# Kernel optimization log

Measured on AMD Instinct MI355X. Metric: run time of the kernel, lower is better.

Reference implementation:

```python
import jax, jax.numpy as jnp
import numpy as np

N_NODES = 100000
N_EDGES = 600000
HID = 128
CH_OUT = 3


def setup_inputs() -> dict:
    key = jax.random.key(0)
    ks = jax.random.split(key, 16)
    s = 0.05  # small init to keep tanh in its linear-ish range
    inp = {
        "x": jax.random.normal(ks[0], (N_NODES, HID), dtype=jnp.float32),
        "pos": jax.random.normal(ks[1], (N_NODES, 3), dtype=jnp.float32),
        "edge_index": jax.random.randint(ks[2], (2, N_EDGES), 0, N_NODES, dtype=jnp.int32),
        "fe_w1": jax.random.normal(ks[3], (2 * HID + 1, HID), dtype=jnp.float32) * s,
        "fe_b1": jnp.zeros((HID,), jnp.float32),
        "fe_w2": jax.random.normal(ks[4], (HID, HID), dtype=jnp.float32) * s,
        "fe_b2": jnp.zeros((HID,), jnp.float32),
        "finf_w": jax.random.normal(ks[5], (HID, 1), dtype=jnp.float32) * s,
        "finf_b": jnp.zeros((1,), jnp.float32),
        "fh_w1": jax.random.normal(ks[6], (2 * HID, HID), dtype=jnp.float32) * s,
        "fh_b1": jnp.zeros((HID,), jnp.float32),
        "fh_w2": jax.random.normal(ks[7], (HID, HID), dtype=jnp.float32) * s,
        "fh_b2": jnp.zeros((HID,), jnp.float32),
        "l1_w": jax.random.normal(ks[8], (HID, HID), dtype=jnp.float32) * s,
        "l1_b": jnp.zeros((HID,), jnp.float32),
        "l2_w": jax.random.normal(ks[9], (HID, HID), dtype=jnp.float32) * s,
        "l2_b": jnp.zeros((HID,), jnp.float32),
        "l3_w": jax.random.normal(ks[10], (HID, HID), dtype=jnp.float32) * s,
        "l3_b": jnp.zeros((HID,), jnp.float32),
        "l4_w": jax.random.normal(ks[11], (HID, HID), dtype=jnp.float32) * s,
        "l4_b": jnp.zeros((HID,), jnp.float32),
        "l5_w": jax.random.normal(ks[12], (HID, CH_OUT), dtype=jnp.float32) * s,
        "l5_b": jnp.zeros((CH_OUT,), jnp.float32),
    }
    return inp


def reference(x, pos, edge_index, fe_w1, fe_b1, fe_w2, fe_b2, finf_w, finf_b,
              fh_w1, fh_b1, fh_w2, fh_b2, l1_w, l1_b, l2_w, l2_b, l3_w, l3_b,
              l4_w, l4_b, l5_w, l5_b):
    e_st, e_end = edge_index[0], edge_index[1]
    # dists = ||(pos_i - pos_j)^2||_2  (norm of the squared difference, as in source)
    d = pos[e_st] - pos[e_end]                                  # [E, 3]
    dists = jnp.linalg.norm(jnp.square(d), axis=1, keepdims=True)  # [E, 1]
    # edge MLP f_e
    tmp = jnp.concatenate([x[e_st], x[e_end], dists], axis=1)   # [E, 2H+1]
    m_ij = jnp.tanh(tmp @ fe_w1 + fe_b1)
    m_ij = jnp.tanh(m_ij @ fe_w2 + fe_b2)                        # [E, H]
    # gating f_inf
    e_ij = jnp.tanh(m_ij @ finf_w + finf_b)                      # [E, 1]
    # scatter-sum to source nodes (index_add on edge_index[0])
    m_i = jax.ops.segment_sum(e_ij * m_ij, e_st, num_segments=x.shape[0])  # [N, H]
    # node update f_h with residual
    h = jnp.concatenate([x, m_i], axis=1)                        # [N, 2H]
    x = x + (jnp.tanh(h @ fh_w1 + fh_b1) @ fh_w2 + fh_b2)
    # dense head (dropout p=0.0 is identity)
    lrelu = lambda v: jax.nn.leaky_relu(v, negative_slope=0.01)
    x = lrelu(x @ l1_w + l1_b)
    x = lrelu(x @ l2_w + l2_b)
    x = lrelu(x @ l3_w + l3_b)
    x = lrelu(x @ l4_w + l4_b)
    return x @ l5_w + l5_b
```

## Files before the change

### kernel.cpp

```cpp
#include <hip/hip_runtime.h>
#include <math.h>

#define HID 128

typedef unsigned short u16;
typedef __attribute__((ext_vector_type(8))) short bfrag;
typedef __attribute__((ext_vector_type(4))) float f32x4;
typedef __attribute__((ext_vector_type(8))) unsigned short u16x8;
typedef __attribute__((ext_vector_type(4))) unsigned short u16x4;

__device__ __forceinline__ float fast_tanh(float v) {
    v = fminf(15.0f, fmaxf(-15.0f, v));
    float e = __expf(2.0f * v);
    float r = __builtin_amdgcn_rcpf(e + 1.0f);
    return 1.0f - 2.0f * r;
}

__device__ __forceinline__ u16 f2b(float f) {
    union { float f; unsigned int u; } v;
    v.f = f;
    unsigned int u = v.u;
    return (u16)((u + 0x7FFFu + ((u >> 16) & 1u)) >> 16);
}
__device__ __forceinline__ float b2f(u16 b) {
    union { unsigned int u; float f; } v;
    v.u = ((unsigned int)b) << 16;
    return v.f;
}
__device__ __forceinline__ float bits2f(unsigned u) {
    union { unsigned u; float f; } v; v.u = u; return v.f;
}

__global__ void __launch_bounds__(256) prep_x(const float* __restrict__ x,
                                              u16* __restrict__ xb) {
    int i = blockIdx.x * 256 + threadIdx.x;
    const float4 v0 = *(const float4*)(x + (size_t)i * 8);
    const float4 v1 = *(const float4*)(x + (size_t)i * 8 + 4);
    u16x8 o = { f2b(v0.x), f2b(v0.y), f2b(v0.z), f2b(v0.w),
                f2b(v1.x), f2b(v1.y), f2b(v1.z), f2b(v1.w) };
    *(u16x8*)(xb + (size_t)i * 8) = o;
}

__global__ void __launch_bounds__(256) prep_weights(
    const float* __restrict__ w1, const float* __restrict__ fh1,
    const float* __restrict__ w2, const float* __restrict__ fh2,
    const float* __restrict__ l1, const float* __restrict__ l2,
    const float* __restrict__ l3, const float* __restrict__ l4,
    u16* __restrict__ w1t, u16* __restrict__ fh1t,
    u16* __restrict__ w2t, u16* __restrict__ fh2t,
    u16* __restrict__ l1t, u16* __restrict__ l2t,
    u16* __restrict__ l3t, u16* __restrict__ l4t)
{
    int b = blockIdx.x, t = threadIdx.x;
    const float* src; u16* dst; int K;
    if (b < 256) {
        K = 256;
        if (b < 128) { src = w1;  dst = w1t; }
        else         { src = fh1; dst = fh1t; b -= 128; }
    } else {
        K = 128;
        int s = (b - 256) >> 6; b = (b - 256) & 63;
        switch (s) {
            case 0:  src = w2;  dst = w2t;  break;
            case 1:  src = fh2; dst = fh2t; break;
            case 2:  src = l1;  dst = l1t;  break;
            case 3:  src = l2;  dst = l2t;  break;
            case 4:  src = l3;  dst = l3t;  break;
            default: src = l4;  dst = l4t;  break;
        }
    }
    int idx = b * 256 + t;
    int k = idx >> 7, n = idx & 127;
    dst[(size_t)n * K + k] = f2b(src[(size_t)k * 128 + n]);
}

__global__ void __launch_bounds__(256) hist_kernel(const int* __restrict__ est,
                                                   int* __restrict__ cnt, int E) {
    int e = blockIdx.x * 256 + threadIdx.x;
    if (e < E) atomicAdd(&cnt[est[e]], 1);
}

__global__ void __launch_bounds__(256) scan1(const int* __restrict__ cnt,
                                             int* __restrict__ scanout,
                                             int* __restrict__ partial, int N) {
    __shared__ int s[256];
    int t = threadIdx.x, b = blockIdx.x, i = b * 256 + t;
    int v = (i < N) ? cnt[i] : 0;
    s[t] = v; __syncthreads();
#pragma unroll
    for (int d = 1; d < 256; d <<= 1) {
        int add = (t >= d) ? s[t - d] : 0;
        __syncthreads();
        s[t] += add;
        __syncthreads();
    }
    if (i < N) scanout[i] = s[t] - v;
    if (t == 255) partial[b] = s[255];
}

__global__ void __launch_bounds__(512) scan2(int* __restrict__ partial, int NB) {
    __shared__ int s[512];
    int t = threadIdx.x;
    int v = (t < NB) ? partial[t] : 0;
    s[t] = v; __syncthreads();
#pragma unroll
    for (int d = 1; d < 512; d <<= 1) {
        int add = (t >= d) ? s[t - d] : 0;
        __syncthreads();
        s[t] += add;
        __syncthreads();
    }
    if (t < NB) partial[t] = s[t] - v;
}

__global__ void __launch_bounds__(256) scan3(const int* __restrict__ scanout,
                                             const int* __restrict__ partial,
                                             int* __restrict__ offs,
                                             int* __restrict__ cur, int N, int E) {
    int t = threadIdx.x, b = blockIdx.x, i = b * 256 + t;
    if (i < N) { int o = scanout[i] + partial[b]; offs[i] = o; cur[i] = o; }
    if (i == 0) offs[N] = E;
}

__global__ void __launch_bounds__(256) reorder_kernel(const int* __restrict__ est,
                                                      const int* __restrict__ eend,
                                                      int* __restrict__ cur,
                                                      int* __restrict__ est_s,
                                                      int* __restrict__ eend_s, int E) {
    int e = blockIdx.x * 256 + threadIdx.x;
    if (e < E) {
        int s = est[e];
        int p = atomicAdd(&cur[s], 1);
        est_s[p]  = s;
        eend_s[p] = eend[e];
    }
}

template<int KD>
__device__ __forceinline__ void gemm_k(const u16* sbuf, const u16* __restrict__ wt,
                                       int w, int l16, int l4g, f32x4 (&acc)[2][2]) {
    const int RS = KD * 2;
#pragma unroll
    for (int k0 = 0; k0 < KD; k0 += 32) {
        const int kb = k0 * 2 + l4g * 16;
        bfrag a0 = *(const bfrag*)((const char*)sbuf +
                    (unsigned)((l16 * RS + kb) ^ ((l16 & 7) << 4)));
        bfrag a1 = *(const bfrag*)((const char*)sbuf +
                    (unsigned)(((16 + l16) * RS + kb) ^ ((l16 & 7) << 4)));
        bfrag b0 = *(const bfrag*)((const char*)wt + (size_t)(32 * w + l16) * RS + kb);
        bfrag b1 = *(const bfrag*)((const char*)wt + (size_t)(32 * w + 16 + l16) * RS + kb);
        acc[0][0] = __builtin_amdgcn_mfma_f32_16x16x32_bf16(a0, b0, acc[0][0], 0, 0, 0);
        acc[0][1] = __builtin_amdgcn_mfma_f32_16x16x32_bf16(a0, b1, acc[0][1], 0, 0, 0);
        acc[1][0] = __builtin_amdgcn_mfma_f32_16x16x32_bf16(a1, b0, acc[1][0], 0, 0, 0);
        acc[1][1] = __builtin_amdgcn_mfma_f32_16x16x32_bf16(a1, b1, acc[1][1], 0, 0, 0);
    }
}

template<int KD>
__device__ __forceinline__ void gemm_sw(const u16* act, const u16* __restrict__ wt,
                                        int w, int l16, int l4g, f32x4 (&acc)[2][2]) {
    const int RS = KD * 2;
#pragma unroll
    for (int k0 = 0; k0 < KD; k0 += 32) {
        const int kb = k0 * 2 + l4g * 16;
        bfrag wa0 = *(const bfrag*)((const char*)wt + (size_t)(32 * w + l16) * RS + kb);
        bfrag wa1 = *(const bfrag*)((const char*)wt + (size_t)(32 * w + 16 + l16) * RS + kb);
        bfrag be0 = *(const bfrag*)((const char*)act +
                    (unsigned)((l16 * RS + kb) ^ ((l16 & 7) << 4)));
        bfrag be1 = *(const bfrag*)((const char*)act +
                    (unsigned)(((16 + l16) * RS + kb) ^ ((l16 & 7) << 4)));
        acc[0][0] = __builtin_amdgcn_mfma_f32_16x16x32_bf16(wa0, be0, acc[0][0], 0, 0, 0);
        acc[0][1] = __builtin_amdgcn_mfma_f32_16x16x32_bf16(wa0, be1, acc[0][1], 0, 0, 0);
        acc[1][0] = __builtin_amdgcn_mfma_f32_16x16x32_bf16(wa1, be0, acc[1][0], 0, 0, 0);
        acc[1][1] = __builtin_amdgcn_mfma_f32_16x16x32_bf16(wa1, be1, acc[1][1], 0, 0, 0);
    }
}

__global__ void __launch_bounds__(256, 2)
egc_edge_csr(const u16* __restrict__ xb, const float* __restrict__ pos,
             const int* __restrict__ est_s, const int* __restrict__ eend_s,
             const u16* __restrict__ w1t, const float* __restrict__ w1last,
             const float* __restrict__ b1, const u16* __restrict__ w2t,
             const float* __restrict__ b2, const float* __restrict__ fw,
             const float* __restrict__ fb, u16* __restrict__ g,
             float* __restrict__ ev, int n_tiles)
{
    __shared__ __attribute__((aligned(16))) u16 a_sh[2][32 * 256];
    __shared__ __attribute__((aligned(16))) u16 m1_sh[32 * 128];
    __shared__ float red[32][17];
    __shared__ float dist_l[2][32];

    const int t = threadIdx.x, lane = t & 63, w = t >> 6;
    const int l16 = lane & 15, l4g = lane >> 4;
    const unsigned swz = (unsigned)((l16 & 7) << 4);

    bfrag wa10[8], wa11[8], w2f0[4], w2f1[4];
#pragma unroll
    for (int i = 0; i < 8; ++i) {
        int kb = i * 64 + l4g * 16;
        wa10[i] = *(const bfrag*)((const char*)w1t + (size_t)(32 * w + l16) * 512 + kb);
        wa11[i] = *(const bfrag*)((const char*)w1t + (size_t)(32 * w + 16 + l16) * 512 + kb);
    }
#pragma unroll
    for (int i = 0; i < 4; ++i) {
        int kb = i * 64 + l4g * 16;
        w2f0[i] = *(const bfrag*)((const char*)w2t + (size_t)(32 * w + l16) * 256 + kb);
        w2f1[i] = *(const bfrag*)((const char*)w2t + (size_t)(32 * w + 16 + l16) * 256 + kb);
    }
    float w1l_r[2][4], b1_r[2][4], b2_r[2][4], fw_r[2][4];
#pragma unroll
    for (int mi = 0; mi < 2; ++mi)
#pragma unroll
        for (int rg = 0; rg < 4; ++rg) {
            int n = 32 * w + 16 * mi + l4g * 4 + rg;
            w1l_r[mi][rg] = w1last[n];
            b1_r[mi][rg]  = b1[n];
            b2_r[mi][rg]  = b2[n];
            fw_r[mi][rg]  = fw[n];
        }
    const float fbv = fb[0];

    float4 sv0, sv1, sv2, sv3;
    float pax = 0, pay = 0, paz = 0, pbx = 0, pby = 0, pbz = 0;

#define EDGE_ISSUE(TILE) do {                                                  \
        int e0_ = (TILE) * 32;                                                 \
        { int f_ = t;       int e_ = f_ >> 5, q_ = f_ & 31; int ge_ = e0_ + e_;\
          int nd_ = (q_ < 16) ? est_s[ge_] : eend_s[ge_];                      \
          sv0 = *(const float4*)(xb + (size_t)nd_ * 128 + (q_ & 15) * 8); }    \
        { int f_ = t + 256; int e_ = f_ >> 5, q_ = f_ & 31; int ge_ = e0_ + e_;\
          int nd_ = (q_ < 16) ? est_s[ge_] : eend_s[ge_];                      \
          sv1 = *(const float4*)(xb + (size_t)nd_ * 128 + (q_ & 15) * 8); }    \
        { int f_ = t + 512; int e_ = f_ >> 5, q_ = f_ & 31; int ge_ = e0_ + e_;\
          int nd_ = (q_ < 16) ? est_s[ge_] : eend_s[ge_];                      \
          sv2 = *(const float4*)(xb + (size_t)nd_ * 128 + (q_ & 15) * 8); }    \
        { int f_ = t + 768; int e_ = f_ >> 5, q_ = f_ & 31; int ge_ = e0_ + e_;\
          int nd_ = (q_ < 16) ? est_s[ge_] : eend_s[ge_];                      \
          sv3 = *(const float4*)(xb + (size_t)nd_ * 128 + (q_ & 15) * 8); }    \
        if (t < 32) {                                                          \
            int ge_ = e0_ + t;                                                 \
            int a_ = est_s[ge_], b_ = eend_s[ge_];                             \
            pax = pos[a_ * 3]; pay = pos[a_ * 3 + 1]; paz = pos[a_ * 3 + 2];   \
            pbx = pos[b_ * 3]; pby = pos[b_ * 3 + 1]; pbz = pos[b_ * 3 + 2];   \
        }                                                                      \
    } while (0)

#define EDGE_COMMIT(BUF) do {                                                  \
        { int f_ = t;       int e_ = f_ >> 5, q_ = f_ & 31;                    \
          unsigned by_ = (unsigned)(e_ * 512 + q_ * 16) ^ (unsigned)((e_ & 7) << 4); \
          *(float4*)((char*)a_sh[BUF] + by_) = sv0; }                          \
        { int f_ = t + 256; int e_ = f_ >> 5, q_ = f_ & 31;                    \
          unsigned by_ = (unsigned)(e_ * 512 + q_ * 16) ^ (unsigned)((e_ & 7) << 4); \
          *(float4*)((char*)a_sh[BUF] + by_) = sv1; }                          \
        { int f_ = t + 512; int e_ = f_ >> 5, q_ = f_ & 31;                    \
          unsigned by_ = (unsigned)(e_ * 512 + q_ * 16) ^ (unsigned)((e_ & 7) << 4); \
          *(float4*)((char*)a_sh[BUF] + by_) = sv2; }                          \
        { int f_ = t + 768; int e_ = f_ >> 5, q_ = f_ & 31;                    \
          unsigned by_ = (unsigned)(e_ * 512 + q_ * 16) ^ (unsigned)((e_ & 7) << 4); \
          *(float4*)((char*)a_sh[BUF] + by_) = sv3; }                          \
        if (t < 32) {                                                          \
            float dx_ = pax - pbx, dy_ = pay - pby, dz_ = paz - pbz;           \
            dx_ *= dx_; dy_ *= dy_; dz_ *= dz_;                                \
            dist_l[BUF][t] = sqrtf(dx_ * dx_ + dy_ * dy_ + dz_ * dz_);         \
        }                                                                      \
    } while (0)

    int tile = blockIdx.x;
    EDGE_ISSUE(tile);
    int buf = 0;

    if (tile < n_tiles)
    while (true) {
        EDGE_COMMIT(buf);
        __syncthreads();
        int next = tile + gridDim.x;
        if (next < n_tiles) EDGE_ISSUE(next);
        const int e0 = tile * 32;

        {
            f32x4 acc[2][2] = {};
#pragma unroll
            for (int i = 0; i < 8; ++i) {
                int kb = i * 64 + l4g * 16;
                bfrag be0 = *(const bfrag*)((const char*)a_sh[buf] +
                            ((unsigned)(l16 * 512 + kb) ^ swz));
                bfrag be1 = *(const bfrag*)((const char*)a_sh[buf] +
                            ((unsigned)((16 + l16) * 512 + kb) ^ swz));
                acc[0][0] = __builtin_amdgcn_mfma_f32_16x16x32_bf16(wa10[i], be0, acc[0][0], 0, 0, 0);
                acc[0][1] = __builtin_amdgcn_mfma_f32_16x16x32_bf16(wa10[i], be1, acc[0][1], 0, 0, 0);
                acc[1][0] = __builtin_amdgcn_mfma_f32_16x16x32_bf16(wa11[i], be0, acc[1][0], 0, 0, 0);
                acc[1][1] = __builtin_amdgcn_mfma_f32_16x16x32_bf16(wa11[i], be1, acc[1][1], 0, 0, 0);
            }
            float de0 = dist_l[buf][l16];
            float de1 = dist_l[buf][16 + l16];
#pragma unroll
            for (int mi = 0; mi < 2; ++mi)
#pragma unroll
                for (int ni = 0; ni < 2; ++ni) {
                    float de = ni ? de1 : de0;
                    u16x4 pk;
#pragma unroll
                    for (int rg = 0; rg < 4; ++rg) {
                        float v = fast_tanh(acc[mi][ni][rg] + de * w1l_r[mi][rg] + b1_r[mi][rg]);
                        pk[rg] = f2b(v);
                    }
                    unsigned byte = ((unsigned)((16 * ni + l16) * 256 +
                                     (32 * w + 16 * mi + l4g * 4) * 2)) ^ swz;
                    *(u16x4*)((char*)m1_sh + byte) = pk;
                }
        }
        __syncthreads();

        {
            f32x4 acc[2][2] = {};
#pragma unroll
            for (int i = 0; i < 4; ++i) {
                int kb = i * 64 + l4g * 16;
                bfrag me0 = *(const bfrag*)((const char*)m1_sh +
                            ((unsigned)(l16 * 256 + kb) ^ swz));
                bfrag me1 = *(const bfrag*)((const char*)m1_sh +
                            ((unsigned)((16 + l16) * 256 + kb) ^ swz));
                acc[0][0] = __builtin_amdgcn_mfma_f32_16x16x32_bf16(w2f0[i], me0, acc[0][0], 0, 0, 0);
                acc[0][1] = __builtin_amdgcn_mfma_f32_16x16x32_bf16(w2f0[i], me1, acc[0][1], 0, 0, 0);
                acc[1][0] = __builtin_amdgcn_mfma_f32_16x16x32_bf16(w2f1[i], me0, acc[1][0], 0, 0, 0);
                acc[1][1] = __builtin_amdgcn_mfma_f32_16x16x32_bf16(w2f1[i], me1, acc[1][1], 0, 0, 0);
            }
            float part0 = 0.0f, part1 = 0.0f;
#pragma unroll
            for (int mi = 0; mi < 2; ++mi)
#pragma unroll
                for (int ni = 0; ni < 2; ++ni) {
                    u16x4 pk;
                    float ps = 0.0f;
#pragma unroll
                    for (int rg = 0; rg < 4; ++rg) {
                        float v = fast_tanh(acc[mi][ni][rg] + b2_r[mi][rg]);
                        ps += v * fw_r[mi][rg];
                        pk[rg] = f2b(v);
                    }
                    if (ni) part1 += ps; else part0 += ps;
                    int dstrow = e0 + 16 * ni + l16;
                    *(u16x4*)(g + (size_t)dstrow * 128 + (32 * w + 16 * mi + l4g * 4)) = pk;
                }
            red[l16][w * 4 + l4g]      = part0;
            red[16 + l16][w * 4 + l4g] = part1;
        }
        __syncthreads();

        if (t < 32) {
            float s = 0.0f;
#pragma unroll
            for (int j = 0; j < 16; ++j) s += red[t][j];
            ev[e0 + t] = fast_tanh(s + fbv);
        }

        tile = next; buf ^= 1;
        if (tile >= n_tiles) break;
    }
#undef EDGE_ISSUE
#undef EDGE_COMMIT
}

__global__ void __launch_bounds__(256, 8)
gather_seq(const u16* __restrict__ g, const float* __restrict__ ev,
           const int* __restrict__ offs, u16* __restrict__ m_i)
{
    const int lane = threadIdx.x & 63;
    const int half = lane >> 5;
    const int l32  = lane & 31;
    const int n = blockIdx.x * 4 + (threadIdx.x >> 6);
    const int beg = offs[n], end = offs[n + 1];
    float a0 = 0.0f, a1 = 0.0f, a2 = 0.0f, a3 = 0.0f;
    for (int e = beg + half; e < end; e += 2) {
        uint2 v = *(const uint2*)(g + (size_t)e * 128 + l32 * 4);
        float ee = ev[e];
        a0 += ee * bits2f(v.x << 16);
        a1 += ee * bits2f(v.x & 0xFFFF0000u);
        a2 += ee * bits2f(v.y << 16);
        a3 += ee * bits2f(v.y & 0xFFFF0000u);
    }
    a0 += __shfl_xor(a0, 32);
    a1 += __shfl_xor(a1, 32);
    a2 += __shfl_xor(a2, 32);
    a3 += __shfl_xor(a3, 32);
    if (half == 0) {
        uint2 o;
        o.x = (unsigned)f2b(a0) | ((unsigned)f2b(a1) << 16);
        o.y = (unsigned)f2b(a2) | ((unsigned)f2b(a3) << 16);
        *(uint2*)(m_i + (size_t)n * 128 + l32 * 4) = o;
    }
}

__global__ void __launch_bounds__(256, 3)
egc_edge_mfma(const u16* __restrict__ xb, const float* __restrict__ pos,
              const int* __restrict__ est, const int* __restrict__ eend,
              const u16* __restrict__ w1t, const float* __restrict__ w1last,
              const float* __restrict__ b1, const u16* __restrict__ w2t,
              const float* __restrict__ b2, const float* __restrict__ fw,
              const float* __restrict__ fb, float* __restrict__ m_i)
{
    __shared__ __attribute__((aligned(16))) u16 a_sh[32 * 256];
    __shared__ __attribute__((aligned(16))) u16 m1_sh[32 * 128];
    __shared__ float m2_sh[32][132];
    __shared__ float dist_l[32];
    __shared__ float ev_l[32];
    __shared__ int   st_l[32];

    const int t = threadIdx.x;
    const int e0 = blockIdx.x * 32;
    const int lane = t & 63;
    const int w = t >> 6;
    const int l16 = lane & 15, l4g = lane >> 4;

#pragma unroll
    for (int i = 0; i < 4; ++i) {
        int f = t + 256 * i;
        int e = f >> 5, q = f & 31;
        int ge = e0 + e;
        int node = (q < 16) ? est[ge] : eend[ge];
        float4 v = *(const float4*)(xb + (size_t)node * 128 + (q & 15) * 8);
        unsigned byte = (unsigned)(e * 512 + q * 16) ^ (unsigned)((e & 7) << 4);
        *(float4*)((char*)a_sh + byte) = v;
    }
    if (t < 32) {
        int ge = e0 + t;
        int a = est[ge], b = eend[ge];
        st_l[t] = a;
        float dx = pos[a * 3 + 0] - pos[b * 3 + 0];
        float dy = pos[a * 3 + 1] - pos[b * 3 + 1];
        float dz = pos[a * 3 + 2] - pos[b * 3 + 2];
        dx *= dx; dy *= dy; dz *= dz;
        dist_l[t] = sqrtf(dx * dx + dy * dy + dz * dz);
    }
    __syncthreads();

    {
        f32x4 acc[2][2] = {};
        gemm_k<256>(a_sh, w1t, w, l16, l4g, acc);
#pragma unroll
        for (int mi = 0; mi < 2; ++mi)
#pragma unroll
            for (int ni = 0; ni < 2; ++ni) {
                const int col = 32 * w + 16 * ni + l16;
                const float wl = w1last[col], bb = b1[col];
#pragma unroll
                for (int rg = 0; rg < 4; ++rg) {
                    const int row = 16 * mi + l4g * 4 + rg;
                    float v = fast_tanh(acc[mi][ni][rg] + dist_l[row] * wl + bb);
                    unsigned byte = (unsigned)((row * 256 + col * 2) ^ ((row & 7) << 4));
                    *(u16*)((char*)m1_sh + byte) = f2b(v);
                }
            }
    }
    __syncthreads();

    {
        f32x4 acc[2][2] = {};
        gemm_k<128>(m1_sh, w2t, w, l16, l4g, acc);
#pragma unroll
        for (int mi = 0; mi < 2; ++mi)
#pragma unroll
            for (int ni = 0; ni < 2; ++ni) {
                const int col = 32 * w + 16 * ni + l16;
                const float bb = b2[col];
#pragma unroll
                for (int rg = 0; rg < 4; ++rg) {
                    const int row = 16 * mi + l4g * 4 + rg;
                    m2_sh[row][col] = fast_tanh(acc[mi][ni][rg] + bb);
                }
            }
    }
    __syncthreads();

    if (t < 128) {
        int e = t >> 2, p = t & 3;
        float s = 0.0f;
#pragma unroll
        for (int k = 0; k < 32; ++k) s += m2_sh[e][p * 32 + k] * fw[p * 32 + k];
        s += __shfl_xor(s, 1);
        s += __shfl_xor(s, 2);
        if (p == 0) ev_l[e] = fast_tanh(s + fb[0]);
    }
    __syncthreads();

    {
        int e = t >> 3, l8 = t & 7;
        float ev = ev_l[e];
        size_t base = (size_t)st_l[e] * HID + l8;
#pragma unroll
        for (int i = 0; i < 16; ++i)
            unsafeAtomicAdd(m_i + base + 8 * i, ev * m2_sh[e][l8 + 8 * i]);
    }
}

#define NODE_LAYER_SW(SRC, KD, WT, BIAS, DST, ACT)                             \
    {                                                                          \
        f32x4 acc[2][2] = {};                                                  \
        gemm_sw<KD>(SRC, WT, w, l16, l4g, acc);                                \
        float bbr[2][4];                                                       \
        _Pragma("unroll")                                                      \
        for (int mi = 0; mi < 2; ++mi)                                         \
            _Pragma("unroll")                                                  \
            for (int rg = 0; rg < 4; ++rg)                                     \
                bbr[mi][rg] = (BIAS)[32 * w + 16 * mi + l4g * 4 + rg];         \
        _Pragma("unroll")                                                      \
        for (int mi = 0; mi < 2; ++mi)                                         \
            _Pragma("unroll")                                                  \
            for (int ni = 0; ni < 2; ++ni) {                                   \
                const int node = 16 * ni + l16;                                \
                const int ch = 32 * w + 16 * mi + l4g * 4;                     \
                u16x4 pk;                                                      \
                _Pragma("unroll")                                              \
                for (int rg = 0; rg < 4; ++rg) {                               \
                    float v = acc[mi][ni][rg] + bbr[mi][rg];                   \
                    ACT;                                                       \
                    pk[rg] = f2b(v);                                           \
                }                                                              \
                unsigned byte = ((unsigned)(node * 256 + ch * 2)) ^ swz;       \
                *(u16x4*)((char*)(DST) + byte) = pk;                           \
            }                                                                  \
    }

template<bool MIBF16>
__global__ void __launch_bounds__(256, 3)
egc_node_mfma(const u16* __restrict__ xb, const float* __restrict__ xf,
              const void* __restrict__ m_i,
              const u16* __restrict__ fh1t, const float* __restrict__ hb1,
              const u16* __restrict__ fh2t, const float* __restrict__ hb2,
              const u16* __restrict__ l1t, const float* __restrict__ l1b,
              const u16* __restrict__ l2t, const float* __restrict__ l2b,
              const u16* __restrict__ l3t, const float* __restrict__ l3b,
              const u16* __restrict__ l4t, const float* __restrict__ l4b,
              const float* __restrict__ l5w, const float* __restrict__ l5b,
              float* __restrict__ out)
{
    __shared__ __attribute__((aligned(16))) u16 a_sh[32 * 256];
    __shared__ __attribute__((aligned(16))) u16 bA[32 * 128];
    __shared__ __attribute__((aligned(16))) u16 bB[32 * 128];
    __shared__ float ff[32][132];

    const int t = threadIdx.x;
    const int n0 = blockIdx.x * 32;
    const int lane = t & 63;
    const int w = t >> 6;
    const int l16 = lane & 15, l4g = lane >> 4;
    const unsigned swz = (unsigned)((l16 & 7) << 4);

#pragma unroll
    for (int i = 0; i < 2; ++i) {
        int f = t + 256 * i;
        int n = f >> 4, q = f & 15;
        float4 v = *(const float4*)(xb + (size_t)(n0 + n) * 128 + q * 8);
        unsigned byte = (unsigned)((n * 512 + q * 16) ^ ((n & 7) << 4));
        *(float4*)((char*)a_sh + byte) = v;
    }
    if (MIBF16) {
#pragma unroll
        for (int i = 0; i < 2; ++i) {
            int f = t + 256 * i;
            int n = f >> 4, q = f & 15;
            float4 v = *(const float4*)((const u16*)m_i + (size_t)(n0 + n) * 128 + q * 8);
            unsigned byte = (unsigned)((n * 512 + 256 + q * 16) ^ ((n & 7) << 4));
            *(float4*)((char*)a_sh + byte) = v;
        }
    } else {
#pragma unroll
        for (int i = 0; i < 2; ++i) {
            int f = t + 256 * i;
            int n = f >> 4, q = f & 15;
            const float* src = (const float*)m_i + (size_t)(n0 + n) * 128 + q * 8;
            float4 v0 = *(const float4*)(src);
            float4 v1 = *(const float4*)(src + 4);
            u16x8 o = { f2b(v0.x), f2b(v0.y), f2b(v0.z), f2b(v0.w),
                        f2b(v1.x), f2b(v1.y), f2b(v1.z), f2b(v1.w) };
            unsigned byte = (unsigned)((n * 512 + 256 + q * 16) ^ ((n & 7) << 4));
            *(u16x8*)((char*)a_sh + byte) = o;
        }
    }
    __syncthreads();

    NODE_LAYER_SW(a_sh, 256, fh1t, hb1, bA, { v = fast_tanh(v); })
    __syncthreads();

    {
        f32x4 acc[2][2] = {};
        gemm_sw<128>(bA, fh2t, w, l16, l4g, acc);
        float bbr[2][4];
#pragma unroll
        for (int mi = 0; mi < 2; ++mi)
#pragma unroll
            for (int rg = 0; rg < 4; ++rg)
                bbr[mi][rg] = hb2[32 * w + 16 * mi + l4g * 4 + rg];
#pragma unroll
        for (int mi = 0; mi < 2; ++mi)
#pragma unroll
            for (int ni = 0; ni < 2; ++ni) {
                const int node = 16 * ni + l16;
                const int ch = 32 * w + 16 * mi + l4g * 4;
                float4 xr = *(const float4*)(xf + (size_t)(n0 + node) * 128 + ch);
                u16x4 pk;
                pk[0] = f2b(acc[mi][ni][0] + bbr[mi][0] + xr.x);
                pk[1] = f2b(acc[mi][ni][1] + bbr[mi][1] + xr.y);
                pk[2] = f2b(acc[mi][ni][2] + bbr[mi][2] + xr.z);
                pk[3] = f2b(acc[mi][ni][3] + bbr[mi][3] + xr.w);
                unsigned byte = ((unsigned)(node * 256 + ch * 2)) ^ swz;
                *(u16x4*)((char*)bB + byte) = pk;
            }
    }
    __syncthreads();

    NODE_LAYER_SW(bB, 128, l1t, l1b, bA, { v = v > 0.0f ? v : 0.01f * v; })
    __syncthreads();
    NODE_LAYER_SW(bA, 128, l2t, l2b, bB, { v = v > 0.0f ? v : 0.01f * v; })
    __syncthreads();
    NODE_LAYER_SW(bB, 128, l3t, l3b, bA, { v = v > 0.0f ? v : 0.01f * v; })
    __syncthreads();

    {
        f32x4 acc[2][2] = {};
        gemm_sw<128>(bA, l4t, w, l16, l4g, acc);
        float bbr[2][4];
#pragma unroll
        for (int mi = 0; mi < 2; ++mi)
#pragma unroll
            for (int rg = 0; rg < 4; ++rg)
                bbr[mi][rg] = l4b[32 * w + 16 * mi + l4g * 4 + rg];
#pragma unroll
        for (int mi = 0; mi < 2; ++mi)
#pragma unroll
            for (int ni = 0; ni < 2; ++ni) {
                const int node = 16 * ni + l16;
                const int ch = 32 * w + 16 * mi + l4g * 4;
                float4 o;
                float v0 = acc[mi][ni][0] + bbr[mi][0];
                float v1 = acc[mi][ni][1] + bbr[mi][1];
                float v2 = acc[mi][ni][2] + bbr[mi][2];
                float v3 = acc[mi][ni][3] + bbr[mi][3];
                o.x = v0 > 0.0f ? v0 : 0.01f * v0;
                o.y = v1 > 0.0f ? v1 : 0.01f * v1;
                o.z = v2 > 0.0f ? v2 : 0.01f * v2;
                o.w = v3 > 0.0f ? v3 : 0.01f * v3;
                *(float4*)(&ff[node][ch]) = o;
            }
    }
    __syncthreads();

    if (t < 96) {
        int n = t / 3, cc = t % 3;
        float s = l5b[cc];
#pragma unroll 8
        for (int k = 0; k < HID; ++k) s += ff[n][k] * l5w[k * 3 + cc];
        out[(size_t)(n0 + n) * 3 + cc] = s;
    }
}

extern "C" void kernel_launch(void* const* d_in, const int* in_sizes, int n_in,
                              void* d_out, int out_size, void* d_ws, size_t ws_size,
                              hipStream_t stream)
{
    const float* x      = (const float*)d_in[0];
    const float* pos    = (const float*)d_in[1];
    const int*   eidx   = (const int*)d_in[2];
    const float* fe_w1  = (const float*)d_in[3];
    const float* fe_b1  = (const float*)d_in[4];
    const float* fe_w2  = (const float*)d_in[5];
    const float* fe_b2  = (const float*)d_in[6];
    const float* finf_w = (const float*)d_in[7];
    const float* finf_b = (const float*)d_in[8];
    const float* fh_w1  = (const float*)d_in[9];
    const float* fh_b1  = (const float*)d_in[10];
    const float* fh_w2  = (const float*)d_in[11];
    const float* fh_b2  = (const float*)d_in[12];
    const float* l1w    = (const float*)d_in[13];
    const float* l1b    = (const float*)d_in[14];
    const float* l2w    = (const float*)d_in[15];
    const float* l2b    = (const float*)d_in[16];
    const float* l3w    = (const float*)d_in[17];
    const float* l3b    = (const float*)d_in[18];
    const float* l4w    = (const float*)d_in[19];
    const float* l4b    = (const float*)d_in[20];
    const float* l5w    = (const float*)d_in[21];
    const float* l5b    = (const float*)d_in[22];
    float* out = (float*)d_out;

    const int n_edges = in_sizes[2] / 2;
    const int n_nodes = in_sizes[0] / HID;
    const int nsb     = (n_nodes + 255) / 256;
    const int n_tiles = n_edges / 32;

    char* ws = (char*)d_ws;
    const bool use_csr = (ws_size >= 208800000ULL);

    if (use_csr) {
        u16* g     = (u16*)(ws + 0);
        u16* xb    = (u16*)(ws + 153600000);
        u16* m_i   = (u16*)(ws + 179200000);
        int* est_s  = (int*)(ws + 179200000);
        int* eend_s = (int*)(ws + 181600000);
        u16* w1t  = (u16*)(ws + 204800000);
        u16* w2t  = (u16*)(ws + 204865536);
        u16* fh1t = (u16*)(ws + 204898304);
        u16* fh2t = (u16*)(ws + 204963840);
        u16* l1t  = (u16*)(ws + 204996608);
        u16* l2t  = (u16*)(ws + 205029376);
        u16* l3t  = (u16*)(ws + 205062144);
        u16* l4t  = (u16*)(ws + 205094912);
        int* cnt  = (int*)(ws + 205127680);
        int* offs = (int*)(ws + 205527680);
        int* cur  = (int*)(ws + 205927696);
        float* ev = (float*)(ws + 206327696);
        int* part = (int*)(ws + 208727696);

        (void)hipMemsetAsync(cnt, 0, (size_t)n_nodes * sizeof(int), stream);
        prep_x<<<dim3((n_nodes * HID) / (256 * 8)), dim3(256), 0, stream>>>(x, xb);
        prep_weights<<<dim3(640), dim3(256), 0, stream>>>(
            fe_w1, fh_w1, fe_w2, fh_w2, l1w, l2w, l3w, l4w,
            w1t, fh1t, w2t, fh2t, l1t, l2t, l3t, l4t);

        hist_kernel<<<dim3((n_edges + 255) / 256), dim3(256), 0, stream>>>(eidx, cnt, n_edges);
        scan1<<<dim3(nsb), dim3(256), 0, stream>>>(cnt, cnt, part, n_nodes);
        scan2<<<dim3(1), dim3(512), 0, stream>>>(part, nsb);
        scan3<<<dim3(nsb), dim3(256), 0, stream>>>(cnt, part, offs, cur, n_nodes, n_edges);
        reorder_kernel<<<dim3((n_edges + 255) / 256), dim3(256), 0, stream>>>(
            eidx, eidx + n_edges, cur, est_s, eend_s, n_edges);

        egc_edge_csr<<<dim3(768), dim3(256), 0, stream>>>(
            xb, pos, est_s, eend_s, w1t, fe_w1 + (size_t)256 * HID, fe_b1,
            w2t, fe_b2, finf_w, finf_b, g, ev, n_tiles);

        gather_seq<<<dim3(n_nodes / 4), dim3(256), 0, stream>>>(g, ev, offs, m_i);

        egc_node_mfma<true><<<dim3(n_nodes / 32), dim3(256), 0, stream>>>(
            xb, x, m_i, fh1t, fh_b1, fh2t, fh_b2, l1t, l1b, l2t, l2b,
            l3t, l3b, l4t, l4b, l5w, l5b, out);
    } else {
        float* m_i = (float*)(ws + 0);
        u16* xb    = (u16*)(ws + 51200000);
        u16* w1t   = (u16*)(ws + 76800000);
        u16* w2t   = (u16*)(ws + 76865536);
        u16* fh1t  = (u16*)(ws + 76898304);
        u16* fh2t  = (u16*)(ws + 76963840);
        u16* l1t   = (u16*)(ws + 76996608);
        u16* l2t   = (u16*)(ws + 77029376);
        u16* l3t   = (u16*)(ws + 77062144);
        u16* l4t   = (u16*)(ws + 77094912);

        (void)hipMemsetAsync(m_i, 0, (size_t)n_nodes * HID * sizeof(float), stream);
        prep_x<<<dim3((n_nodes * HID) / (256 * 8)), dim3(256), 0, stream>>>(x, xb);
        prep_weights<<<dim3(640), dim3(256), 0, stream>>>(
            fe_w1, fh_w1, fe_w2, fh_w2, l1w, l2w, l3w, l4w,
            w1t, fh1t, w2t, fh2t, l1t, l2t, l3t, l4t);

        egc_edge_mfma<<<dim3(n_edges / 32), dim3(256), 0, stream>>>(
            xb, pos, eidx, eidx + n_edges, w1t, fe_w1 + (size_t)256 * HID, fe_b1,
            w2t, fe_b2, finf_w, finf_b, m_i);

        egc_node_mfma<false><<<dim3(n_nodes / 32), dim3(256), 0, stream>>>(
            xb, x, m_i, fh1t, fh_b1, fh2t, fh_b2, l1t, l1b, l2t, l2b,
            l3t, l3b, l4t, l4b, l5w, l5b, out);
    }
}
```

Measured before the change: 393.8 us.

## Merge prep kernels, fuse final projection into layer-4 epilogue, tweak edge grid

Folds the x conversion, weight transposition and edge histogram into one launch to cut kernel launch overhead. Computes the final 3-channel projection as per-lane partial dot products in the last layer's epilogue and reduces 16 partials per output, replacing a 128-wide shared-memory staging loop. Drops the tanh input clamp, switches bf16 rounding to the library intrinsic, and lowers the CSR edge kernel grid from 768 to 512 blocks. Removing the clamp risks overflow of exp for large inputs (it saturates to correct limits though).

```diff
diff --git a/kernel.cpp b/kernel.cpp
--- a/kernel.cpp
+++ b/kernel.cpp
@@ -1,4 +1,5 @@
 #include <hip/hip_runtime.h>
+#include <hip/hip_bf16.h>
 #include <math.h>
 
 #define HID 128
@@ -10,38 +11,21 @@
 typedef __attribute__((ext_vector_type(4))) unsigned short u16x4;
 
 __device__ __forceinline__ float fast_tanh(float v) {
-    v = fminf(15.0f, fmaxf(-15.0f, v));
     float e = __expf(2.0f * v);
     float r = __builtin_amdgcn_rcpf(e + 1.0f);
     return 1.0f - 2.0f * r;
 }
 
 __device__ __forceinline__ u16 f2b(float f) {
-    union { float f; unsigned int u; } v;
-    v.f = f;
-    unsigned int u = v.u;
-    return (u16)((u + 0x7FFFu + ((u >> 16) & 1u)) >> 16);
-}
-__device__ __forceinline__ float b2f(u16 b) {
-    union { unsigned int u; float f; } v;
-    v.u = ((unsigned int)b) << 16;
-    return v.f;
+    __hip_bfloat16 h = __float2bfloat16(f);
+    return *(u16*)&h;
 }
 __device__ __forceinline__ float bits2f(unsigned u) {
     union { unsigned u; float f; } v; v.u = u; return v.f;
 }
 
-__global__ void __launch_bounds__(256) prep_x(const float* __restrict__ x,
-                                              u16* __restrict__ xb) {
-    int i = blockIdx.x * 256 + threadIdx.x;
-    const float4 v0 = *(const float4*)(x + (size_t)i * 8);
-    const float4 v1 = *(const float4*)(x + (size_t)i * 8 + 4);
-    u16x8 o = { f2b(v0.x), f2b(v0.y), f2b(v0.z), f2b(v0.w),
-                f2b(v1.x), f2b(v1.y), f2b(v1.z), f2b(v1.w) };
-    *(u16x8*)(xb + (size_t)i * 8) = o;
-}
-
-__global__ void __launch_bounds__(256) prep_weights(
+__global__ void __launch_bounds__(256) prep_combo(
+    const float* __restrict__ x, u16* __restrict__ xb,
     const float* __restrict__ w1, const float* __restrict__ fh1,
     const float* __restrict__ w2, const float* __restrict__ fh2,
     const float* __restrict__ l1, const float* __restrict__ l2,
@@ -49,34 +33,45 @@
     u16* __restrict__ w1t, u16* __restrict__ fh1t,
     u16* __restrict__ w2t, u16* __restrict__ fh2t,
     u16* __restrict__ l1t, u16* __restrict__ l2t,
-    u16* __restrict__ l3t, u16* __restrict__ l4t)
+    u16* __restrict__ l3t, u16* __restrict__ l4t,
+    const int* __restrict__ est, int* __restrict__ cnt, int E, int nxb)
 {
     int b = blockIdx.x, t = threadIdx.x;
-    const float* src; u16* dst; int K;
-    if (b < 256) {
-        K = 256;
-        if (b < 128) { src = w1;  dst = w1t; }
-        else         { src = fh1; dst = fh1t; b -= 128; }
-    } else {
-        K = 128;
-        int s = (b - 256) >> 6; b = (b - 256) & 63;
-        switch (s) {
-            case 0:  src = w2;  dst = w2t;  break;
-            case 1:  src = fh2; dst = fh2t; break;
-            case 2:  src = l1;  dst = l1t;  break;
-            case 3:  src = l2;  dst = l2t;  break;
-            case 4:  src = l3;  dst = l3t;  break;
-            default: src = l4;  dst = l4t;  break;
+    if (b < nxb) {
+        int i = b * 256 + t;
+        const float4 v0 = *(const float4*)(x + (size_t)i * 8);
+        const float4 v1 = *(const float4*)(x + (size_t)i * 8 + 4);
+        u16x8 o = { f2b(v0.x), f2b(v0.y), f2b(v0.z), f2b(v0.w),
+                    f2b(v1.x), f2b(v1.y), f2b(v1.z), f2b(v1.w) };
+        *(u16x8*)(xb + (size_t)i * 8) = o;
+        return;
+    }
+    b -= nxb;
+    if (b < 640) {
+        const float* src; u16* dst; int K;
+        if (b < 256) {
+            K = 256;
+            if (b < 128) { src = w1;  dst = w1t; }
+            else         { src = fh1; dst = fh1t; b -= 128; }
+        } else {
+            K = 128;
+            int s = (b - 256) >> 6; b = (b - 256) & 63;
+            switch (s) {
+                case 0:  src = w2;  dst = w2t;  break;
+                case 1:  src = fh2; dst = fh2t; break;
+                case 2:  src = l1;  dst = l1t;  break;
+                case 3:  src = l2;  dst = l2t;  break;
+                case 4:  src = l3;  dst = l3t;  break;
+                default: src = l4;  dst = l4t;  break;
+            }
         }
-    }
-    int idx = b * 256 + t;
-    int k = idx >> 7, n = idx & 127;
-    dst[(size_t)n * K + k] = f2b(src[(size_t)k * 128 + n]);
-}
-
-__global__ void __launch_bounds__(256) hist_kernel(const int* __restrict__ est,
-                                                   int* __restrict__ cnt, int E) {
-    int e = blockIdx.x * 256 + threadIdx.x;
+        int idx = b * 256 + t;
+        int k = idx >> 7, n = idx & 127;
+        dst[(size_t)n * K + k] = f2b(src[(size_t)k * 128 + n]);
+        return;
+    }
+    b -= 640;
+    int e = b * 256 + t;
     if (e < E) atomicAdd(&cnt[est[e]], 1);
 }
 
@@ -521,7 +516,7 @@
             }                                                                  \
     }
 
-template<bool MIBF16>
+template<int MODE>
 __global__ void __launch_bounds__(256, 3)
 egc_node_mfma(const u16* __restrict__ xb, const float* __restrict__ xf,
               const void* __restrict__ m_i,
@@ -537,7 +532,7 @@
     __shared__ __attribute__((aligned(16))) u16 a_sh[32 * 256];
     __shared__ __attribute__((aligned(16))) u16 bA[32 * 128];
     __shared__ __attribute__((aligned(16))) u16 bB[32 * 128];
-    __shared__ float ff[32][132];
+    __shared__ float red[32][3][17];
 
     const int t = threadIdx.x;
     const int n0 = blockIdx.x * 32;
@@ -554,7 +549,7 @@
         unsigned byte = (unsigned)((n * 512 + q * 16) ^ ((n & 7) << 4));
         *(float4*)((char*)a_sh + byte) = v;
     }
-    if (MIBF16) {
+    if (MODE == 0) {
 #pragma unroll
         for (int i = 0; i < 2; ++i) {
             int f = t + 256 * i;
@@ -619,37 +614,42 @@
     {
         f32x4 acc[2][2] = {};
         gemm_sw<128>(bA, l4t, w, l16, l4g, acc);
-        float bbr[2][4];
+        float bbr[2][4], w5[2][4][3];
 #pragma unroll
         for (int mi = 0; mi < 2; ++mi)
 #pragma unroll
-            for (int rg = 0; rg < 4; ++rg)
-                bbr[mi][rg] = l4b[32 * w + 16 * mi + l4g * 4 + rg];
-#pragma unroll
-        for (int mi = 0; mi < 2; ++mi)
-#pragma unroll
-            for (int ni = 0; ni < 2; ++ni) {
-                const int node = 16 * ni + l16;
-                const int ch = 32 * w + 16 * mi + l4g * 4;
-                float4 o;
-                float v0 = acc[mi][ni][0] + bbr[mi][0];
-                float v1 = acc[mi][ni][1] + bbr[mi][1];
-                float v2 = acc[mi][ni][2] + bbr[mi][2];
-                float v3 = acc[mi][ni][3] + bbr[mi][3];
-                o.x = v0 > 0.0f ? v0 : 0.01f * v0;
-                o.y = v1 > 0.0f ? v1 : 0.01f * v1;
-                o.z = v2 > 0.0f ? v2 : 0.01f * v2;
-                o.w = v3 > 0.0f ? v3 : 0.01f * v3;
-                *(float4*)(&ff[node][ch]) = o;
+            for (int rg = 0; rg < 4; ++rg) {
+                int ch = 32 * w + 16 * mi + l4g * 4 + rg;
+                bbr[mi][rg] = l4b[ch];
+#pragma unroll
+                for (int cc = 0; cc < 3; ++cc) w5[mi][rg][cc] = l5w[ch * 3 + cc];
             }
+#pragma unroll
+        for (int ni = 0; ni < 2; ++ni) {
+            float p0 = 0.0f, p1 = 0.0f, p2 = 0.0f;
+#pragma unroll
+            for (int mi = 0; mi < 2; ++mi)
+#pragma unroll
+                for (int rg = 0; rg < 4; ++rg) {
+                    float v = acc[mi][ni][rg] + bbr[mi][rg];
+                    v = v > 0.0f ? v : 0.01f * v;
+                    p0 += v * w5[mi][rg][0];
+                    p1 += v * w5[mi][rg][1];
+                    p2 += v * w5[mi][rg][2];
+                }
+            const int n = 16 * ni + l16, j = w * 4 + l4g;
+            red[n][0][j] = p0;
+            red[n][1][j] = p1;
+            red[n][2][j] = p2;
+        }
     }
     __syncthreads();
 
     if (t < 96) {
         int n = t / 3, cc = t % 3;
         float s = l5b[cc];
-#pragma unroll 8
-        for (int k = 0; k < HID; ++k) s += ff[n][k] * l5w[k * 3 + cc];
+#pragma unroll
+        for (int j = 0; j < 16; ++j) s += red[n][cc][j];
         out[(size_t)(n0 + n) * 3 + cc] = s;
     }
 }
@@ -687,6 +687,8 @@
     const int n_nodes = in_sizes[0] / HID;
     const int nsb     = (n_nodes + 255) / 256;
     const int n_tiles = n_edges / 32;
+    const int nxb     = (n_nodes * HID) / (256 * 8);
+    const int nhb     = (n_edges + 255) / 256;
 
     char* ws = (char*)d_ws;
     const bool use_csr = (ws_size >= 208800000ULL);
@@ -712,25 +714,23 @@
         int* part = (int*)(ws + 208727696);
 
         (void)hipMemsetAsync(cnt, 0, (size_t)n_nodes * sizeof(int), stream);
-        prep_x<<<dim3((n_nodes * HID) / (256 * 8)), dim3(256), 0, stream>>>(x, xb);
-        prep_weights<<<dim3(640), dim3(256), 0, stream>>>(
-            fe_w1, fh_w1, fe_w2, fh_w2, l1w, l2w, l3w, l4w,
-            w1t, fh1t, w2t, fh2t, l1t, l2t, l3t, l4t);
-
-        hist_kernel<<<dim3((n_edges + 255) / 256), dim3(256), 0, stream>>>(eidx, cnt, n_edges);
+        prep_combo<<<dim3(nxb + 640 + nhb), dim3(256), 0, stream>>>(
+            x, xb, fe_w1, fh_w1, fe_w2, fh_w2, l1w, l2w, l3w, l4w,
+            w1t, fh1t, w2t, fh2t, l1t, l2t, l3t, l4t, eidx, cnt, n_edges, nxb);
+
         scan1<<<dim3(nsb), dim3(256), 0, stream>>>(cnt, cnt, part, n_nodes);
         scan2<<<dim3(1), dim3(512), 0, stream>>>(part, nsb);
         scan3<<<dim3(nsb), dim3(256), 0, stream>>>(cnt, part, offs, cur, n_nodes, n_edges);
-        reorder_kernel<<<dim3((n_edges + 255) / 256), dim3(256), 0, stream>>>(
+        reorder_kernel<<<dim3(nhb), dim3(256), 0, stream>>>(
             eidx, eidx + n_edges, cur, est_s, eend_s, n_edges);
 
-        egc_edge_csr<<<dim3(768), dim3(256), 0, stream>>>(
+        egc_edge_csr<<<dim3(512), dim3(256), 0, stream>>>(
             xb, pos, est_s, eend_s, w1t, fe_w1 + (size_t)256 * HID, fe_b1,
             w2t, fe_b2, finf_w, finf_b, g, ev, n_tiles);
 
         gather_seq<<<dim3(n_nodes / 4), dim3(256), 0, stream>>>(g, ev, offs, m_i);
 
-        egc_node_mfma<true><<<dim3(n_nodes / 32), dim3(256), 0, stream>>>(
+        egc_node_mfma<0><<<dim3(n_nodes / 32), dim3(256), 0, stream>>>(
             xb, x, m_i, fh1t, fh_b1, fh2t, fh_b2, l1t, l1b, l2t, l2b,
             l3t, l3b, l4t, l4b, l5w, l5b, out);
     } else {
@@ -746,16 +746,15 @@
         u16* l4t   = (u16*)(ws + 77094912);
 
         (void)hipMemsetAsync(m_i, 0, (size_t)n_nodes * HID * sizeof(float), stream);
-        prep_x<<<dim3((n_nodes * HID) / (256 * 8)), dim3(256), 0, stream>>>(x, xb);
-        prep_weights<<<dim3(640), dim3(256), 0, stream>>>(
-            fe_w1, fh_w1, fe_w2, fh_w2, l1w, l2w, l3w, l4w,
-            w1t, fh1t, w2t, fh2t, l1t, l2t, l3t, l4t);
+        prep_combo<<<dim3(nxb + 640), dim3(256), 0, stream>>>(
+            x, xb, fe_w1, fh_w1, fe_w2, fh_w2, l1w, l2w, l3w, l4w,
+            w1t, fh1t, w2t, fh2t, l1t, l2t, l3t, l4t, eidx, (int*)d_ws, 0, nxb);
 
         egc_edge_mfma<<<dim3(n_edges / 32), dim3(256), 0, stream>>>(
             xb, pos, eidx, eidx + n_edges, w1t, fe_w1 + (size_t)256 * HID, fe_b1,
             w2t, fe_b2, finf_w, finf_b, m_i);
 
-        egc_node_mfma<false><<<dim3(n_nodes / 32), dim3(256), 0, stream>>>(
+        egc_node_mfma<1><<<dim3(n_nodes / 32), dim3(256), 0, stream>>>(
             xb, x, m_i, fh1t, fh_b1, fh2t, fh_b2, l1t, l1b, l2t, l2b,
             l3t, l3b, l4t, l4b, l5w, l5b, out);
     }
```

New measurement: 358.5 us. 9.0% less time.
